# Optimization experiments

Hardware: AMD Instinct MI355X
Metric: run time of the kernel (lower is better)

## Reference

```python
import jax, jax.numpy as jnp
import numpy as np


def setup_inputs() -> dict:
    key = jax.random.key(0)
    k1, k2, k3, k4 = jax.random.split(key, 4)
    B, T, C, H = 16, 2048, 1024, 128
    x = jax.random.normal(k1, (B, T, C), dtype=jnp.float32)
    # bias-free Dense kernels (stored as [in, out] like keras)
    s = 1.0 / np.sqrt(C)
    Wk = jax.random.normal(k2, (C, H), dtype=jnp.float32) * s
    Wq = jax.random.normal(k3, (C, H), dtype=jnp.float32) * s
    Wv = jax.random.normal(k4, (C, H), dtype=jnp.float32) * s
    return {"x": x, "Wk": Wk, "Wq": Wq, "Wv": Wv}


def reference(x, Wk, Wq, Wv):
    # single-head causal self-attention (dropout inactive at inference)
    B, T, C = x.shape
    H = Wk.shape[-1]
    k = jnp.einsum('btc,ch->bth', x, Wk)   # [B,T,H]
    q = jnp.einsum('btc,ch->bth', x, Wq)
    v = jnp.einsum('btc,ch->bth', x, Wv)
    scale = 1.0 / jnp.sqrt(jnp.float32(H))
    wei = jnp.einsum('bqh,bkh->bqk', q, k) * scale          # [B,T,T]
    causal = jnp.tril(jnp.ones((T, T), dtype=bool))
    wei = jnp.where(causal, wei, -jnp.inf)
    wei = jax.nn.softmax(wei, axis=-1)
    out = jnp.einsum('bqk,bkh->bqh', wei, v)                # [B,T,H]
    return out
```

## Files before the change

kernel.cpp:

```cpp
#include <hip/hip_runtime.h>
#include <hip/hip_bf16.h>

typedef __bf16 bf16x8_t __attribute__((ext_vector_type(8)));
typedef __bf16 bf16x4_t __attribute__((ext_vector_type(4)));
typedef float  f32x4_t  __attribute__((ext_vector_type(4)));

#define MFMA_16x16x32_BF16(A, B, C) __builtin_amdgcn_mfma_f32_16x16x32_bf16((A), (B), (C), 0, 0, 0)

static constexpr int B_ = 16;
static constexpr int T_ = 2048;
static constexpr int C_ = 1024;
static constexpr int H_ = 128;
static constexpr long M_ = (long)B_ * T_;

__device__ __forceinline__ void gload_lds16(const void* g, void* l)
{
    __builtin_amdgcn_global_load_lds(
        (const __attribute__((address_space(1))) void*)g,
        (__attribute__((address_space(3))) void*)l, 16, 0, 0);
}

__global__ __launch_bounds__(128) void wt_kernel(
    const float* __restrict__ Wq, const float* __restrict__ Wk,
    const float* __restrict__ Wv, __bf16* __restrict__ WT)
{
    const int z = blockIdx.y;
    const float* __restrict__ W = (z == 0) ? Wq : (z == 1) ? Wk : Wv;
    const int h  = threadIdx.x;
    const int c0 = blockIdx.x * 8;
    bf16x8_t v;
    #pragma unroll
    for (int j = 0; j < 8; ++j)
        v[j] = (__bf16)W[(c0 + j) * H_ + h];
    *(bf16x8_t*)&WT[((long)z * H_ + h) * C_ + c0] = v;
}

__global__ __launch_bounds__(512, 2) void proj_kernel(
    const float*  __restrict__ x,
    const __bf16* __restrict__ WT,
    __bf16* __restrict__ qo,
    __bf16* __restrict__ ko,
    __bf16* __restrict__ vo)
{
    __shared__ float  XS[3][128 * 32];
    __shared__ __bf16 WS[3][384 * 32];

    const int tid  = threadIdx.x;
    const int w    = tid >> 6;
    const int lane = tid & 63;
    const int m16  = lane & 15;
    const int quad = lane >> 4;
    const int wm   = w >> 2;
    const int wn   = w & 3;

    const long r0 = (long)blockIdx.x * 128;

    const int xl_row = lane >> 3;
    const int xl_u   = (lane & 7) ^ xl_row;
    const int wl_row = lane >> 2;
    const int wl_u   = (lane & 3) ^ ((lane >> 3) & 3);

    f32x4_t acc[4][6];
    #pragma unroll
    for (int hh = 0; hh < 4; ++hh)
        #pragma unroll
        for (int j = 0; j < 6; ++j) acc[hh][j] = f32x4_t{0, 0, 0, 0};

#define ISSUE(T, BUF)                                                        \
    {                                                                        \
        const int k0_ = (T) * 32;                                            \
        _Pragma("unroll")                                                    \
        for (int ch = 0; ch < 2; ++ch) {                                     \
            const int rb = w * 8 + ch * 64;                                  \
            gload_lds16(&x[(r0 + rb + xl_row) * C_ + k0_ + xl_u * 4],        \
                        &XS[BUF][rb * 32]);                                  \
        }                                                                    \
        _Pragma("unroll")                                                    \
        for (int ch = 0; ch < 3; ++ch) {                                     \
            const int rb = w * 48 + ch * 16;                                 \
            gload_lds16(&WT[(long)(rb + wl_row) * C_ + k0_ + wl_u * 8],      \
                        &WS[BUF][rb * 32]);                                  \
        }                                                                    \
    }

    ISSUE(0, 0);
    ISSUE(1, 1);
    asm volatile("s_waitcnt vmcnt(5)" ::: "memory");
    __builtin_amdgcn_sched_barrier(0);
    __builtin_amdgcn_s_barrier();
    __builtin_amdgcn_sched_barrier(0);

    const int asw = m16 & 7;
    const int qsw = (quad ^ ((m16 >> 1) & 3)) << 3;

    for (int t = 0; t < 32; ++t) {
        const int cur = t % 3;
        if (t + 2 < 32) ISSUE(t + 2, (t + 2) % 3);
        __builtin_amdgcn_sched_barrier(0);

        bf16x8_t a[4];
        #pragma unroll
        for (int hh = 0; hh < 4; ++hh) {
            const int row = wm * 64 + hh * 16 + m16;
            f32x4_t lo = *(const f32x4_t*)&XS[cur][row * 32 + (((quad * 2 + 0) ^ asw) << 2)];
            f32x4_t hi = *(const f32x4_t*)&XS[cur][row * 32 + (((quad * 2 + 1) ^ asw) << 2)];
            #pragma unroll
            for (int jj = 0; jj < 4; ++jj) {
                a[hh][jj]     = (__bf16)lo[jj];
                a[hh][4 + jj] = (__bf16)hi[jj];
            }
        }
        #pragma unroll
        for (int j = 0; j < 6; ++j) {
            const int row = wn * 96 + j * 16 + m16;
            bf16x8_t b = *(const bf16x8_t*)&WS[cur][row * 32 + qsw];
            #pragma unroll
            for (int hh = 0; hh < 4; ++hh)
                acc[hh][j] = MFMA_16x16x32_BF16(a[hh], b, acc[hh][j]);
        }

        __builtin_amdgcn_sched_barrier(0);
        if (t + 2 < 32) asm volatile("s_waitcnt vmcnt(5)" ::: "memory");
        else            asm volatile("s_waitcnt vmcnt(0)" ::: "memory");
        asm volatile("s_waitcnt lgkmcnt(0)" ::: "memory");
        __builtin_amdgcn_s_barrier();
        __builtin_amdgcn_sched_barrier(0);
    }
#undef ISSUE

    #pragma unroll
    for (int hh = 0; hh < 4; ++hh) {
        const long rbase = r0 + wm * 64 + hh * 16 + quad * 4;
        #pragma unroll
        for (int j = 0; j < 6; ++j) {
            const int nt = wn * 6 + j;
            const int z  = nt >> 3;
            const int h  = (nt & 7) * 16 + m16;
            if (z < 2) {
                __bf16* __restrict__ o = z ? ko : qo;
                #pragma unroll
                for (int r = 0; r < 4; ++r)
                    o[(rbase + r) * H_ + h] = (__bf16)acc[hh][j][r];
            } else {
                long bb = rbase >> 11, tt = rbase & 2047;
                bf16x4_t pk;
                #pragma unroll
                for (int r = 0; r < 4; ++r) pk[r] = (__bf16)acc[hh][j][r];
                *(bf16x4_t*)&vo[bb * (H_ * (long)T_) + h * (long)T_ + tt] = pk;
            }
        }
    }
}

__global__ __launch_bounds__(256) void attn_kernel(
    const __bf16* __restrict__ q,
    const __bf16* __restrict__ k,
    const __bf16* __restrict__ vT,
    float* __restrict__ out)
{
    __shared__ __bf16 KS[64 * 136];
    __shared__ __bf16 VS[128 * 72];
    __shared__ __bf16 PS[4][16 * 72];

    const int L   = blockIdx.x;
    const int b   = L & 15;
    const int Lh  = L >> 4;
    const int qb  = (Lh < 16) ? (31 - Lh) : (Lh - 16);

    const int tid  = threadIdx.x;
    const int w    = tid >> 6;
    const int lane = tid & 63;
    const int m16  = lane & 15;
    const int quad = lane >> 4;
    const int koff = quad * 8;

    const __bf16* __restrict__ qp = q  + (long)b * T_ * H_;
    const __bf16* __restrict__ kp = k  + (long)b * T_ * H_;
    const __bf16* __restrict__ vp = vT + (long)b * H_ * T_;

    const int q0w = qb * 64 + w * 16;
    const int qg  = q0w + m16;

    bf16x8_t qfr[4];
    #pragma unroll
    for (int s = 0; s < 4; ++s)
        qfr[s] = *(const bf16x8_t*)&qp[(q0w + m16) * H_ + s * 32 + koff];

    f32x4_t acc[8];
    #pragma unroll
    for (int i = 0; i < 8; ++i) acc[i] = f32x4_t{0, 0, 0, 0};
    float mrun = -1e30f, lrun = 0.f;

    __bf16* Pb = &PS[w][0];
    const float SC = 0.08838834764831845f;
    const int kend = qb * 64 + 64;

    const int krow = tid >> 4, kc16 = tid & 15;
    const int vrow = tid >> 3, vc8  = tid & 7;

    for (int tk0 = 0; tk0 < kend; tk0 += 64) {
        __syncthreads();
        #pragma unroll
        for (int ch = 0; ch < 4; ++ch) {
            int r = krow + ch * 16;
            *(bf16x8_t*)&KS[r * 136 + kc16 * 8] =
                *(const bf16x8_t*)&kp[(tk0 + r) * H_ + kc16 * 8];
        }
        #pragma unroll
        for (int ch = 0; ch < 4; ++ch) {
            int hh = vrow + ch * 32;
            *(bf16x8_t*)&VS[hh * 72 + vc8 * 8] =
                *(const bf16x8_t*)&vp[hh * (long)T_ + tk0 + vc8 * 8];
        }
        __syncthreads();

        f32x4_t st[4];
        #pragma unroll
        for (int kt = 0; kt < 4; ++kt) {
            f32x4_t s = f32x4_t{0, 0, 0, 0};
            #pragma unroll
            for (int sI = 0; sI < 4; ++sI) {
                bf16x8_t kf = *(const bf16x8_t*)&KS[(kt * 16 + m16) * 136 + sI * 32 + koff];
                s = MFMA_16x16x32_BF16(kf, qfr[sI], s);
            }
            st[kt] = s;
        }

        float vv[4][4];
        if (tk0 + 63 <= q0w) {
            #pragma unroll
            for (int kt = 0; kt < 4; ++kt)
                #pragma unroll
                for (int r = 0; r < 4; ++r)
                    vv[kt][r] = st[kt][r] * SC;
        } else {
            #pragma unroll
            for (int kt = 0; kt < 4; ++kt)
                #pragma unroll
                for (int r = 0; r < 4; ++r) {
                    int kg = tk0 + kt * 16 + quad * 4 + r;
                    vv[kt][r] = (kg <= qg) ? st[kt][r] * SC : -1e30f;
                }
        }

        float mloc = -1e30f;
        #pragma unroll
        for (int kt = 0; kt < 4; ++kt)
            #pragma unroll
            for (int r = 0; r < 4; ++r)
                mloc = fmaxf(mloc, vv[kt][r]);
        mloc = fmaxf(mloc, __shfl_xor(mloc, 16, 64));
        mloc = fmaxf(mloc, __shfl_xor(mloc, 32, 64));

        float mnew = fmaxf(mrun, mloc);
        float al   = __expf(mrun - mnew);
        float psum = 0.f;
        #pragma unroll
        for (int kt = 0; kt < 4; ++kt) {
            bf16x4_t pk;
            #pragma unroll
            for (int r = 0; r < 4; ++r) {
                float p = __expf(vv[kt][r] - mnew);
                psum += p;
                pk[r] = (__bf16)p;
            }
            *(bf16x4_t*)&Pb[m16 * 72 + kt * 16 + quad * 4] = pk;
        }
        psum += __shfl_xor(psum, 16, 64);
        psum += __shfl_xor(psum, 32, 64);
        mrun = mnew;
        lrun = lrun * al + psum;

        #pragma unroll
        for (int i = 0; i < 8; ++i)
            #pragma unroll
            for (int r = 0; r < 4; ++r)
                acc[i][r] *= al;

        #pragma unroll
        for (int half = 0; half < 2; ++half) {
            bf16x8_t pa = *(const bf16x8_t*)&Pb[m16 * 72 + half * 32 + koff];
            #pragma unroll
            for (int i = 0; i < 8; ++i) {
                bf16x8_t vf = *(const bf16x8_t*)&VS[(i * 16 + m16) * 72 + half * 32 + koff];
                acc[i] = MFMA_16x16x32_BF16(vf, pa, acc[i]);
            }
        }
    }

    float* __restrict__ ob = out + (long)b * T_ * H_;
    const float inv = 1.f / lrun;
    #pragma unroll
    for (int i = 0; i < 8; ++i) {
        f32x4_t o;
        #pragma unroll
        for (int r = 0; r < 4; ++r) o[r] = acc[i][r] * inv;
        *(f32x4_t*)&ob[(q0w + m16) * H_ + i * 16 + quad * 4] = o;
    }
}

extern "C" void kernel_launch(void* const* d_in, const int* in_sizes, int n_in,
                              void* d_out, int out_size, void* d_ws, size_t ws_size,
                              hipStream_t stream)
{
    const float* x  = (const float*)d_in[0];
    const float* Wk = (const float*)d_in[1];
    const float* Wq = (const float*)d_in[2];
    const float* Wv = (const float*)d_in[3];

    __bf16* qws = (__bf16*)d_ws;
    __bf16* kws = qws + M_ * H_;
    __bf16* vws = kws + M_ * H_;
    __bf16* WT  = vws + (long)B_ * H_ * T_;
    float*  out = (float*)d_out;

    wt_kernel  <<<dim3(C_ / 8, 3), 128, 0, stream>>>(Wq, Wk, Wv, WT);
    proj_kernel<<<dim3((int)(M_ / 128)), 512, 0, stream>>>(x, WT, qws, kws, vws);
    attn_kernel<<<dim3(512), 256, 0, stream>>>(qws, kws, vws, out);
}
```

Baseline: 276.5 us.

## Shrink projection tiles to 64x192 with double buffering and more blocks

The QKV projection kernel moves from 512-thread blocks computing 128 rows x 384 outputs with a triple-buffered async pipeline to 256-thread blocks computing 64 rows x 192 outputs with plain double buffering and __syncthreads. The grid grows fourfold, which raises block count and occupancy (4 blocks per CU) and shrinks the LDS per block. In exchange, x rows are now loaded twice (once per column half), per-block reuse drops, and the explicit vmcnt-based prefetch depth is lost.

```diff
diff --git a/kernel.cpp b/kernel.cpp
--- a/kernel.cpp
+++ b/kernel.cpp
@@ -35,34 +35,37 @@
     *(bf16x8_t*)&WT[((long)z * H_ + h) * C_ + c0] = v;
 }
 
-__global__ __launch_bounds__(512, 2) void proj_kernel(
+__global__ __launch_bounds__(256, 4) void proj_kernel(
     const float*  __restrict__ x,
     const __bf16* __restrict__ WT,
     __bf16* __restrict__ qo,
     __bf16* __restrict__ ko,
     __bf16* __restrict__ vo)
 {
-    __shared__ float  XS[3][128 * 32];
-    __shared__ __bf16 WS[3][384 * 32];
+    __shared__ float  XS[2][64 * 32];
+    __shared__ __bf16 WS[2][192 * 32];
 
     const int tid  = threadIdx.x;
     const int w    = tid >> 6;
     const int lane = tid & 63;
     const int m16  = lane & 15;
     const int quad = lane >> 4;
-    const int wm   = w >> 2;
-    const int wn   = w & 3;
-
-    const long r0 = (long)blockIdx.x * 128;
+    const int wr   = w >> 1;
+    const int wc   = w & 1;
+
+    const int  rb = blockIdx.x >> 1;
+    const int  cb = blockIdx.x & 1;
+    const long r0 = (long)rb * 64;
+    const int  n0 = cb * 192;
 
     const int xl_row = lane >> 3;
     const int xl_u   = (lane & 7) ^ xl_row;
     const int wl_row = lane >> 2;
     const int wl_u   = (lane & 3) ^ ((lane >> 3) & 3);
 
-    f32x4_t acc[4][6];
-    #pragma unroll
-    for (int hh = 0; hh < 4; ++hh)
+    f32x4_t acc[2][6];
+    #pragma unroll
+    for (int hh = 0; hh < 2; ++hh)
         #pragma unroll
         for (int j = 0; j < 6; ++j) acc[hh][j] = f32x4_t{0, 0, 0, 0};
 
@@ -71,37 +74,32 @@
         const int k0_ = (T) * 32;                                            \
         _Pragma("unroll")                                                    \
         for (int ch = 0; ch < 2; ++ch) {                                     \
-            const int rb = w * 8 + ch * 64;                                  \
-            gload_lds16(&x[(r0 + rb + xl_row) * C_ + k0_ + xl_u * 4],        \
-                        &XS[BUF][rb * 32]);                                  \
+            const int rbx = w * 16 + ch * 8;                                 \
+            gload_lds16(&x[(r0 + rbx + xl_row) * C_ + k0_ + xl_u * 4],       \
+                        &XS[BUF][rbx * 32]);                                 \
         }                                                                    \
         _Pragma("unroll")                                                    \
         for (int ch = 0; ch < 3; ++ch) {                                     \
-            const int rb = w * 48 + ch * 16;                                 \
-            gload_lds16(&WT[(long)(rb + wl_row) * C_ + k0_ + wl_u * 8],      \
-                        &WS[BUF][rb * 32]);                                  \
+            const int rbw = w * 48 + ch * 16;                                \
+            gload_lds16(&WT[(long)(n0 + rbw + wl_row) * C_ + k0_ + wl_u * 8],\
+                        &WS[BUF][rbw * 32]);                                 \
         }                                                                    \
     }
 
     ISSUE(0, 0);
-    ISSUE(1, 1);
-    asm volatile("s_waitcnt vmcnt(5)" ::: "memory");
-    __builtin_amdgcn_sched_barrier(0);
-    __builtin_amdgcn_s_barrier();
-    __builtin_amdgcn_sched_barrier(0);
+    __syncthreads();
 
     const int asw = m16 & 7;
     const int qsw = (quad ^ ((m16 >> 1) & 3)) << 3;
 
     for (int t = 0; t < 32; ++t) {
-        const int cur = t % 3;
-        if (t + 2 < 32) ISSUE(t + 2, (t + 2) % 3);
-        __builtin_amdgcn_sched_barrier(0);
-
-        bf16x8_t a[4];
-        #pragma unroll
-        for (int hh = 0; hh < 4; ++hh) {
-            const int row = wm * 64 + hh * 16 + m16;
+        const int cur = t & 1;
+        if (t < 31) ISSUE(t + 1, cur ^ 1);
+
+        bf16x8_t a[2];
+        #pragma unroll
+        for (int hh = 0; hh < 2; ++hh) {
+            const int row = wr * 32 + hh * 16 + m16;
             f32x4_t lo = *(const f32x4_t*)&XS[cur][row * 32 + (((quad * 2 + 0) ^ asw) << 2)];
             f32x4_t hi = *(const f32x4_t*)&XS[cur][row * 32 + (((quad * 2 + 1) ^ asw) << 2)];
             #pragma unroll
@@ -112,28 +110,23 @@
         }
         #pragma unroll
         for (int j = 0; j < 6; ++j) {
-            const int row = wn * 96 + j * 16 + m16;
+            const int row = wc * 96 + j * 16 + m16;
             bf16x8_t b = *(const bf16x8_t*)&WS[cur][row * 32 + qsw];
             #pragma unroll
-            for (int hh = 0; hh < 4; ++hh)
+            for (int hh = 0; hh < 2; ++hh)
                 acc[hh][j] = MFMA_16x16x32_BF16(a[hh], b, acc[hh][j]);
         }
 
-        __builtin_amdgcn_sched_barrier(0);
-        if (t + 2 < 32) asm volatile("s_waitcnt vmcnt(5)" ::: "memory");
-        else            asm volatile("s_waitcnt vmcnt(0)" ::: "memory");
-        asm volatile("s_waitcnt lgkmcnt(0)" ::: "memory");
-        __builtin_amdgcn_s_barrier();
-        __builtin_amdgcn_sched_barrier(0);
+        __syncthreads();
     }
 #undef ISSUE
 
     #pragma unroll
-    for (int hh = 0; hh < 4; ++hh) {
-        const long rbase = r0 + wm * 64 + hh * 16 + quad * 4;
+    for (int hh = 0; hh < 2; ++hh) {
+        const long rbase = r0 + wr * 32 + hh * 16 + quad * 4;
         #pragma unroll
         for (int j = 0; j < 6; ++j) {
-            const int nt = wn * 6 + j;
+            const int nt = cb * 12 + wc * 6 + j;
             const int z  = nt >> 3;
             const int h  = (nt & 7) * 16 + m16;
             if (z < 2) {
@@ -315,6 +308,6 @@
     float*  out = (float*)d_out;
 
     wt_kernel  <<<dim3(C_ / 8, 3), 128, 0, stream>>>(Wq, Wk, Wv, WT);
-    proj_kernel<<<dim3((int)(M_ / 128)), 512, 0, stream>>>(x, WT, qws, kws, vws);
+    proj_kernel<<<dim3((int)(M_ / 64) * 2), 256, 0, stream>>>(x, WT, qws, kws, vws);
     attn_kernel<<<dim3(512), 256, 0, stream>>>(qws, kws, vws, out);
 }
```

After: 300.0 us. +8.5%, slower.

## Split attention KV range across two blocks and merge partial softmax results

Applied to the files above, without the earlier changes.

Each query block's causal key range is now split in half across two workgroups (split-K / flash-decoding style), doubling the grid from 512 to 1024 blocks. Each half writes unnormalized fp32 partial outputs plus running max and sum, and a new merge kernel combines them with log-sum-exp rescaling. The aim is more parallelism and better load balance across the CUs. The cost is an extra kernel launch and roughly 2x32 MB of fp32 partial-output traffic written and read back.

```diff
diff --git a/kernel.cpp b/kernel.cpp
--- a/kernel.cpp
+++ b/kernel.cpp
@@ -156,16 +156,20 @@
     const __bf16* __restrict__ q,
     const __bf16* __restrict__ k,
     const __bf16* __restrict__ vT,
-    float* __restrict__ out)
+    float* __restrict__ Opart,
+    float* __restrict__ mpart,
+    float* __restrict__ lpart)
 {
     __shared__ __bf16 KS[64 * 136];
     __shared__ __bf16 VS[128 * 72];
     __shared__ __bf16 PS[4][16 * 72];
 
-    const int L   = blockIdx.x;
-    const int b   = L & 15;
-    const int Lh  = L >> 4;
-    const int qb  = (Lh < 16) ? (31 - Lh) : (Lh - 16);
+    const int bid  = blockIdx.x;
+    const int half = bid & 1;
+    const int L    = bid >> 1;
+    const int b    = L & 15;
+    const int Lh   = L >> 4;
+    const int qb   = (Lh < 16) ? (31 - Lh) : (Lh - 16);
 
     const int tid  = threadIdx.x;
     const int w    = tid >> 6;
@@ -193,12 +197,17 @@
 
     __bf16* Pb = &PS[w][0];
     const float SC = 0.08838834764831845f;
-    const int kend = qb * 64 + 64;
+
+    const int ntile = qb + 1;
+    const int n0    = (ntile + 1) >> 1;
+    const int tt0   = half ? n0 : 0;
+    const int tt1   = half ? ntile : n0;
 
     const int krow = tid >> 4, kc16 = tid & 15;
     const int vrow = tid >> 3, vc8  = tid & 7;
 
-    for (int tk0 = 0; tk0 < kend; tk0 += 64) {
+    for (int tt = tt0; tt < tt1; ++tt) {
+        const int tk0 = tt * 64;
         __syncthreads();
         #pragma unroll
         for (int ch = 0; ch < 4; ++ch) {
@@ -278,25 +287,44 @@
                 acc[i][r] *= al;
 
         #pragma unroll
-        for (int half = 0; half < 2; ++half) {
-            bf16x8_t pa = *(const bf16x8_t*)&Pb[m16 * 72 + half * 32 + koff];
+        for (int hf = 0; hf < 2; ++hf) {
+            bf16x8_t pa = *(const bf16x8_t*)&Pb[m16 * 72 + hf * 32 + koff];
             #pragma unroll
             for (int i = 0; i < 8; ++i) {
-                bf16x8_t vf = *(const bf16x8_t*)&VS[(i * 16 + m16) * 72 + half * 32 + koff];
+                bf16x8_t vf = *(const bf16x8_t*)&VS[(i * 16 + m16) * 72 + hf * 32 + koff];
                 acc[i] = MFMA_16x16x32_BF16(vf, pa, acc[i]);
             }
         }
     }
 
-    float* __restrict__ ob = out + (long)b * T_ * H_;
-    const float inv = 1.f / lrun;
-    #pragma unroll
-    for (int i = 0; i < 8; ++i) {
-        f32x4_t o;
-        #pragma unroll
-        for (int r = 0; r < 4; ++r) o[r] = acc[i][r] * inv;
-        *(f32x4_t*)&ob[(q0w + m16) * H_ + i * 16 + quad * 4] = o;
-    }
+    float* __restrict__ ob = Opart + ((long)half * B_ + b) * T_ * H_;
+    #pragma unroll
+    for (int i = 0; i < 8; ++i)
+        *(f32x4_t*)&ob[(q0w + m16) * H_ + i * 16 + quad * 4] = acc[i];
+    if (quad == 0) {
+        const long rix = (long)half * M_ + (long)b * T_ + q0w + m16;
+        mpart[rix] = mrun;
+        lpart[rix] = lrun;
+    }
+}
+
+__global__ __launch_bounds__(256) void merge_kernel(
+    const float* __restrict__ Opart, const float* __restrict__ mpart,
+    const float* __restrict__ lpart, float* __restrict__ out)
+{
+    const long idx = (long)blockIdx.x * 256 + threadIdx.x;
+    const long row = idx >> 5;
+    const float m0 = mpart[row], m1 = mpart[M_ + row];
+    const float l0 = lpart[row], l1 = lpart[M_ + row];
+    const float m  = fmaxf(m0, m1);
+    const float a0 = __expf(m0 - m), a1 = __expf(m1 - m);
+    const float inv = 1.f / (a0 * l0 + a1 * l1);
+    f32x4_t o0 = *(const f32x4_t*)&Opart[idx * 4];
+    f32x4_t o1 = *(const f32x4_t*)&Opart[(long)M_ * H_ + idx * 4];
+    f32x4_t o;
+    #pragma unroll
+    for (int r = 0; r < 4; ++r) o[r] = (a0 * o0[r] + a1 * o1[r]) * inv;
+    *(f32x4_t*)&out[idx * 4] = o;
 }
 
 extern "C" void kernel_launch(void* const* d_in, const int* in_sizes, int n_in,
@@ -312,9 +340,13 @@
     __bf16* kws = qws + M_ * H_;
     __bf16* vws = kws + M_ * H_;
     __bf16* WT  = vws + (long)B_ * H_ * T_;
+    float*  Opart = (float*)(WT + 3L * H_ * C_);
+    float*  mpart = Opart + 2L * M_ * H_;
+    float*  lpart = mpart + 2L * M_;
     float*  out = (float*)d_out;
 
-    wt_kernel  <<<dim3(C_ / 8, 3), 128, 0, stream>>>(Wq, Wk, Wv, WT);
-    proj_kernel<<<dim3((int)(M_ / 128)), 512, 0, stream>>>(x, WT, qws, kws, vws);
-    attn_kernel<<<dim3(512), 256, 0, stream>>>(qws, kws, vws, out);
-}
+    wt_kernel   <<<dim3(C_ / 8, 3), 128, 0, stream>>>(Wq, Wk, Wv, WT);
+    proj_kernel <<<dim3((int)(M_ / 128)), 512, 0, stream>>>(x, WT, qws, kws, vws);
+    attn_kernel <<<dim3(1024), 256, 0, stream>>>(qws, kws, vws, Opart, mpart, lpart);
+    merge_kernel<<<dim3((int)(M_ * H_ / 4 / 256)), 256, 0, stream>>>(Opart, mpart, lpart, out);
+}
```

Result: no change. 273.5 us (-1.1%).
